# Performance work log

Hardware: AMD Instinct MI355X
Metric: run time of the kernel (lower is better)

Reference implementation:

```python
import math
import jax, jax.numpy as jnp
import numpy as np

SIZE = 5
MUL = 16                      # multiplicity of 0e and 1o in irreps_in and irreps_out
DIM = 4 * MUL                 # 16x0e (16) + 16x1o (48) = 64
INV_SQRT3 = 1.0 / math.sqrt(3.0)          # nonzero entries of wigner_3j for (1,1,0),(0,1,1),(1,0,1)
ALPHA_0 = math.sqrt(1.0 / (2 * MUL))      # out 0e: ir.dim=1 / (two uvw paths, 16*1 elements each)
ALPHA_1 = math.sqrt(3.0 / (2 * MUL))      # out 1o: ir.dim=3 / (two uvw paths, 16*1 elements each)


def _lattice():
    # torch.linspace(-1,1,size), meshgrid 'ij'; steps=(1,1,1) keeps the full cube
    r = np.linspace(-1.0, 1.0, SIZE, dtype=np.float32)
    gx, gy, gz = np.meshgrid(r, r, r, indexing='ij')
    lat = np.stack([gx, gy, gz], axis=-1)                      # (S,S,S,3), order (x,y,z)
    d = np.linalg.norm(lat, axis=-1)
    unit = np.where(d[..., None] > 0, lat / np.maximum(d[..., None], 1e-12), 0.0)
    # e3nn spherical harmonics, normalize=True, 'component' norm; l=1 basis order (y,z,x)
    sh0 = np.ones_like(d)                                      # l=0 component-normalized
    sh1 = math.sqrt(3.0) * unit[..., [1, 2, 0]]                # (S,S,S,3)
    return jnp.asarray(d), jnp.asarray(sh0), jnp.asarray(sh1)


def soft_one_hot_linspace(x, start, end, number):
    sigma = (end - start) / (number - 1)
    values = jnp.linspace(start, end, number, dtype=x.dtype)
    return jnp.exp(-(((x[..., None] - values) / sigma) ** 2)) / 1.12


def setup_inputs() -> dict:
    key = jax.random.key(0)
    k1, k2, k3, k4 = jax.random.split(key, 4)
    return {
        'x': jax.random.normal(k1, (2, DIM, 64, 64, 64), dtype=jnp.float32),
        'lin_w0': jax.random.normal(k2, (MUL, MUL), dtype=jnp.float32),
        'lin_w1': jax.random.normal(k3, (MUL, MUL), dtype=jnp.float32),
        'tp_weight': jax.random.normal(k4, (SIZE, 4 * MUL * MUL), dtype=jnp.float32),
    }


def reference(x, lin_w0, lin_w1, tp_weight):
    d, sh0, sh1 = _lattice()
    B, _, X, Y, Z = x.shape

    # ---- self connection: e3nn Linear per irrep, scaled by 1/sqrt(fan_in) ----
    inv = 1.0 / math.sqrt(MUL)
    x0 = x[:, :MUL]                                            # (B,16,X,Y,Z) scalars
    x1 = x[:, MUL:].reshape(B, MUL, 3, X, Y, Z)                # (B,16,3,X,Y,Z) vectors
    sc0 = jnp.einsum('uw,buxyz->bwxyz', lin_w0, x0) * inv
    sc1 = jnp.einsum('uw,buixyz->bwixyz', lin_w1, x1) * inv
    sc = jnp.concatenate([sc0, sc1.reshape(B, 3 * MUL, X, Y, Z)], axis=1)

    # ---- radial weights: soft one-hot embedding @ learned weights ----
    emb = soft_one_hot_linspace(d, 0.0, 1.0, SIZE) @ tp_weight                 # (S,S,S,1024)
    emb = emb * (jnp.cos(math.pi * d) / SIZE ** 1.5)[..., None]
    mm = MUL * MUL
    wA = emb[..., 0 * mm:1 * mm].reshape(SIZE, SIZE, SIZE, MUL, MUL)  # 0e(x)0e->0e
    wB = emb[..., 1 * mm:2 * mm].reshape(SIZE, SIZE, SIZE, MUL, MUL)  # 0e(x)1o->1o
    wC = emb[..., 2 * mm:3 * mm].reshape(SIZE, SIZE, SIZE, MUL, MUL)  # 1o(x)0e->1o
    wD = emb[..., 3 * mm:4 * mm].reshape(SIZE, SIZE, SIZE, MUL, MUL)  # 1o(x)1o->0e

    # ---- tp.right(sh, weight): kernel (S,S,S, in_dim, out_dim) ----
    eye3 = jnp.eye(3, dtype=x.dtype)
    k00 = ALPHA_0 * wA * sh0[..., None, None]                                        # (g,16,16)
    k10 = (ALPHA_0 * INV_SQRT3) * jnp.einsum('...uw,...i->...uiw', wD, sh1)          # (g,16,3,16)
    k01 = (ALPHA_1 * INV_SQRT3) * jnp.einsum('...uw,...k->...uwk', wB, sh1)          # (g,16,16,3)
    k11 = (ALPHA_1 * INV_SQRT3) * jnp.einsum('...uw,ik->...uiwk',
                                             wC * sh0[..., None, None], eye3)        # (g,16,3,16,3)
    g = (SIZE, SIZE, SIZE)
    top = jnp.concatenate([k00, k01.reshape(*g, MUL, 3 * MUL)], axis=-1)             # (g,16,64)
    bot = jnp.concatenate([k10.reshape(*g, 3 * MUL, MUL),
                           k11.reshape(*g, 3 * MUL, 3 * MUL)], axis=-1)              # (g,48,64)
    kernel = jnp.concatenate([top, bot], axis=-2)                                     # (S,S,S,64,64)

    # einsum('xyzio->oixyz') then conv3d (cross-correlation, same as torch)
    kernel_oi = jnp.transpose(kernel, (4, 3, 0, 1, 2))
    p = SIZE // 2
    conv = jax.lax.conv_general_dilated(
        x, kernel_oi, window_strides=(1, 1, 1), padding=[(p, p)] * 3,
        dimension_numbers=('NCDHW', 'OIDHW', 'NCDHW'))
    return sc + 0.1 * conv
```

## Files before the change

### kernel.cpp

```cpp
#include <hip/hip_runtime.h>
#include <hip/hip_bf16.h>
#include <math.h>

typedef __bf16 bf16x8 __attribute__((ext_vector_type(8)));
typedef __bf16 bf16x2 __attribute__((ext_vector_type(2)));
typedef float  f32x4  __attribute__((ext_vector_type(4)));

#define CI_STRIDE 262144
#define B_STRIDE  16777216
#define Z2 68
#define CP 40

__global__ __launch_bounds__(256) void gen_w(const float* __restrict__ tp,
                                             const float* __restrict__ lw0,
                                             const float* __restrict__ lw1,
                                             __bf16* __restrict__ Wb) {
    const int t  = blockIdx.x;
    const int dx = t / 25, dy = (t / 5) % 5, dz = t % 5;
    const float rx = -1.f + 0.5f * (float)dx;
    const float ry = -1.f + 0.5f * (float)dy;
    const float rz = -1.f + 0.5f * (float)dz;
    const float d    = sqrtf(rx * rx + ry * ry + rz * rz);
    const float invd = (d > 0.f) ? (1.f / d) : 0.f;
    const float SQRT3 = 1.7320508075688772f;
    const float sh1_0 = SQRT3 * ry * invd;
    const float sh1_1 = SQRT3 * rz * invd;
    const float sh1_2 = SQRT3 * rx * invd;
    float basis[5];
#pragma unroll
    for (int m = 0; m < 5; ++m) {
        float u = (d - 0.25f * (float)m) * 4.0f;
        basis[m] = expf(-u * u) * (1.0f / 1.12f);
    }
    const float S  = cosf(3.14159265358979323846f * d) * (1.0f / 11.180339887498949f);
    const float fA = 0.1f * 0.17677669529663687f * S;
    const float fB = 0.1f * 0.3061862178478972f * 0.5773502691896258f * S;
    const float fC = 0.1f * 0.17677669529663687f * 0.5773502691896258f * S;
    const float fD = fB;

    for (int e = threadIdx.x; e < 4096; e += 256) {
        const int co = e >> 6, ci = e & 63;
        int   tt;
        float f;
        if (ci < 16) {
            if (co < 16) { tt = ci * 16 + co; f = fA; }
            else {
                const int c = co - 16, w = c / 3, kk = c % 3;
                tt = 256 + ci * 16 + w;
                f  = fB * ((kk == 0) ? sh1_0 : (kk == 1) ? sh1_1 : sh1_2);
            }
        } else {
            const int a = ci - 16, uu = a / 3, ii = a % 3;
            const float s1i = (ii == 0) ? sh1_0 : (ii == 1) ? sh1_1 : sh1_2;
            if (co < 16) { tt = 768 + uu * 16 + co; f = fC * s1i; }
            else {
                const int c = co - 16, w = c / 3, kk = c % 3;
                tt = 512 + uu * 16 + w;
                f  = (ii == kk) ? fD : 0.0f;
            }
        }
        float E = 0.f;
#pragma unroll
        for (int m = 0; m < 5; ++m) E += basis[m] * tp[m * 1024 + tt];
        float val = f * E;
        if (t == 62) {
            if (ci < 16 && co < 16) {
                val += 0.25f * lw0[ci * 16 + co];
            } else if (ci >= 16 && co >= 16) {
                const int a = co - 16, bq = ci - 16;
                const int wq = a / 3, iq = a % 3, uq = bq / 3, iiq = bq % 3;
                if (iq == iiq) val += 0.25f * lw1[uq * 16 + wq];
            }
        }
        Wb[((size_t)(t * 2 + (ci >> 5)) * 64 + co) * 32 + (ci & 31)] = (__bf16)val;
    }
}

__global__ __launch_bounds__(512, 2) void conv_mfma(const float* __restrict__ x,
                                                    const __bf16* __restrict__ Wb,
                                                    float* __restrict__ out) {
    __shared__ __align__(16) __bf16 xs[20 * Z2 * CP];
    const int tid = threadIdx.x;
    const int l = tid & 63, w = tid >> 6;
    const int q = l >> 4, i16 = l & 15;
    const int b  = blockIdx.x >> 8;
    const int xc = (blockIdx.x >> 2) & 63;
    const int y0 = (blockIdx.x & 3) << 4;

    f32x4 acc[4][8];
#pragma unroll
    for (int mt = 0; mt < 4; ++mt)
#pragma unroll
        for (int nt = 0; nt < 8; ++nt) acc[mt][nt] = (f32x4)(0.f);

    for (int idx = tid; idx < 20 * 4 * CP; idx += 512) {
        const int r = idx / (4 * CP), rem = idx % (4 * CP);
        const int zs = rem / CP, ci = rem % CP;
        const int zp = (zs < 2) ? zs : (64 + zs);
        xs[((size_t)r * Z2 + zp) * CP + ci] = (__bf16)0.f;
    }

    const float* xb = x + (size_t)b * B_STRIDE;

    bf16x8 Acur[4], Anext[4];
#pragma unroll
    for (int mt = 0; mt < 4; ++mt)
        Acur[mt] = *(const bf16x8*)(Wb + ((size_t)(mt * 16 + i16)) * 32 + q * 8);

    for (int h = 0; h < 2; ++h) {
        for (int dx = 0; dx < 5; ++dx) {
            __syncthreads();
            {
                const int xp = xc + dx - 2;
                const bool xok = (xp >= 0) && (xp < 64);
                for (int r = w; r < 20; r += 8) {
                    const int yp = y0 + r - 2;
                    const bool ok = xok && (yp >= 0) && (yp < 64);
                    const float* src = xb + (size_t)(h * 32) * CI_STRIDE
                                     + (size_t)xp * 4096 + yp * 64 + l;
                    __bf16* dst = xs + ((size_t)r * Z2 + 2 + l) * CP;
                    if (ok) {
#pragma unroll
                        for (int ci = 0; ci < 32; ci += 2) {
                            const float a0 = src[(size_t)ci * CI_STRIDE];
                            const float a1 = src[(size_t)(ci + 1) * CI_STRIDE];
                            bf16x2 pk = {(__bf16)a0, (__bf16)a1};
                            *(bf16x2*)(dst + ci) = pk;
                        }
                    } else {
                        bf16x2 zz = {(__bf16)0.f, (__bf16)0.f};
#pragma unroll
                        for (int ci = 0; ci < 32; ci += 2) *(bf16x2*)(dst + ci) = zz;
                    }
                }
            }
            __syncthreads();

            for (int dydz = 0; dydz < 25; ++dydz) {
                const int t = dx * 25 + dydz;
                const int s = h * 125 + t;
                {
                    const int sn = (s < 249) ? (s + 1) : s;
                    const int hn = sn / 125, tn = sn % 125;
                    const __bf16* wp = Wb + ((size_t)(tn * 2 + hn) * 64 + i16) * 32 + q * 8;
#pragma unroll
                    for (int mt = 0; mt < 4; ++mt)
                        Anext[mt] = *(const bf16x8*)(wp + (size_t)mt * 16 * 32);
                }
                const int dy = dydz / 5, dz = dydz % 5;
                const __bf16* bbase = xs + ((size_t)(2 * w + dy) * Z2 + dz + i16) * CP + q * 8;
                bf16x8 Bf[8];
#pragma unroll
                for (int yy = 0; yy < 2; ++yy)
#pragma unroll
                    for (int zt = 0; zt < 4; ++zt)
                        Bf[yy * 4 + zt] = *(const bf16x8*)(bbase + (size_t)(yy * Z2 + zt * 16) * CP);
#pragma unroll
                for (int mt = 0; mt < 4; ++mt)
#pragma unroll
                    for (int nt = 0; nt < 8; ++nt)
                        acc[mt][nt] = __builtin_amdgcn_mfma_f32_16x16x32_bf16(
                            Acur[mt], Bf[nt], acc[mt][nt], 0, 0, 0);
#pragma unroll
                for (int mt = 0; mt < 4; ++mt) Acur[mt] = Anext[mt];
            }
        }
    }

    const size_t ob = (size_t)b * B_STRIDE + (size_t)xc * 4096;
#pragma unroll
    for (int mt = 0; mt < 4; ++mt)
#pragma unroll
        for (int j = 0; j < 4; ++j) {
            const int co = mt * 16 + q * 4 + j;
            float* op = out + ob + (size_t)co * CI_STRIDE;
#pragma unroll
            for (int nt = 0; nt < 8; ++nt) {
                const int y = y0 + 2 * w + (nt >> 2);
                const int z = (nt & 3) * 16 + i16;
                op[y * 64 + z] = acc[mt][nt][j];
            }
        }
}

extern "C" void kernel_launch(void* const* d_in, const int* in_sizes, int n_in,
                              void* d_out, int out_size, void* d_ws, size_t ws_size,
                              hipStream_t stream) {
    (void)in_sizes; (void)n_in; (void)out_size; (void)ws_size;
    const float* x   = (const float*)d_in[0];
    const float* lw0 = (const float*)d_in[1];
    const float* lw1 = (const float*)d_in[2];
    const float* tp  = (const float*)d_in[3];
    float* out = (float*)d_out;
    __bf16* Wb = (__bf16*)d_ws;

    gen_w<<<125, 256, 0, stream>>>(tp, lw0, lw1, Wb);
    conv_mfma<<<512, 512, 0, stream>>>(x, Wb, out);
}
```

Before: 570.2 us.

## Halve conv block to 4 waves over 8 y-rows, vectorize staging, raise MFMA priority

The conv kernel now launches 1024 blocks of 256 threads, each covering 8 y-rows with a 12-row LDS halo instead of 16 rows with a 20-row halo. This doubles the block count and shrinks LDS per block, which should help occupancy and load balance. The cost is a larger halo fraction and more redundant global reads. Staging now packs 8 channels into one 16-byte LDS store, and s_setprio is raised around the MFMA loop so compute waves are favoured over loaders.

Measured after the change: 567.5 us. Within noise of the previous version (-0.5%).

```diff
diff --git a/kernel.cpp b/kernel.cpp
--- a/kernel.cpp
+++ b/kernel.cpp
@@ -10,6 +10,7 @@
 #define B_STRIDE  16777216
 #define Z2 68
 #define CP 40
+#define NROW 12
 
 __global__ __launch_bounds__(256) void gen_w(const float* __restrict__ tp,
                                              const float* __restrict__ lw0,
@@ -76,16 +77,16 @@
     }
 }
 
-__global__ __launch_bounds__(512, 2) void conv_mfma(const float* __restrict__ x,
+__global__ __launch_bounds__(256, 2) void conv_mfma(const float* __restrict__ x,
                                                     const __bf16* __restrict__ Wb,
                                                     float* __restrict__ out) {
-    __shared__ __align__(16) __bf16 xs[20 * Z2 * CP];
+    __shared__ __align__(16) __bf16 xs[NROW * Z2 * CP];
     const int tid = threadIdx.x;
     const int l = tid & 63, w = tid >> 6;
     const int q = l >> 4, i16 = l & 15;
-    const int b  = blockIdx.x >> 8;
-    const int xc = (blockIdx.x >> 2) & 63;
-    const int y0 = (blockIdx.x & 3) << 4;
+    const int b  = blockIdx.x >> 9;
+    const int xc = (blockIdx.x >> 3) & 63;
+    const int y0 = (blockIdx.x & 7) << 3;
 
     f32x4 acc[4][8];
 #pragma unroll
@@ -93,11 +94,13 @@
 #pragma unroll
         for (int nt = 0; nt < 8; ++nt) acc[mt][nt] = (f32x4)(0.f);
 
-    for (int idx = tid; idx < 20 * 4 * CP; idx += 512) {
-        const int r = idx / (4 * CP), rem = idx % (4 * CP);
-        const int zs = rem / CP, ci = rem % CP;
+    if (tid < NROW * 4 * 4) {
+        const int r = tid >> 4, rem = tid & 15;
+        const int zs = rem >> 2, c8 = (rem & 3) << 3;
         const int zp = (zs < 2) ? zs : (64 + zs);
-        xs[((size_t)r * Z2 + zp) * CP + ci] = (__bf16)0.f;
+        bf16x8 zz = {(__bf16)0.f, (__bf16)0.f, (__bf16)0.f, (__bf16)0.f,
+                     (__bf16)0.f, (__bf16)0.f, (__bf16)0.f, (__bf16)0.f};
+        *(bf16x8*)(xs + ((size_t)r * Z2 + zp) * CP + c8) = zz;
     }
 
     const float* xb = x + (size_t)b * B_STRIDE;
@@ -113,7 +116,7 @@
             {
                 const int xp = xc + dx - 2;
                 const bool xok = (xp >= 0) && (xp < 64);
-                for (int r = w; r < 20; r += 8) {
+                for (int r = w; r < NROW; r += 4) {
                     const int yp = y0 + r - 2;
                     const bool ok = xok && (yp >= 0) && (yp < 64);
                     const float* src = xb + (size_t)(h * 32) * CI_STRIDE
@@ -121,16 +124,18 @@
                     __bf16* dst = xs + ((size_t)r * Z2 + 2 + l) * CP;
                     if (ok) {
 #pragma unroll
-                        for (int ci = 0; ci < 32; ci += 2) {
-                            const float a0 = src[(size_t)ci * CI_STRIDE];
-                            const float a1 = src[(size_t)(ci + 1) * CI_STRIDE];
-                            bf16x2 pk = {(__bf16)a0, (__bf16)a1};
-                            *(bf16x2*)(dst + ci) = pk;
+                        for (int c0 = 0; c0 < 32; c0 += 8) {
+                            bf16x8 pk;
+#pragma unroll
+                            for (int j = 0; j < 8; ++j)
+                                pk[j] = (__bf16)src[(size_t)(c0 + j) * CI_STRIDE];
+                            *(bf16x8*)(dst + c0) = pk;
                         }
                     } else {
-                        bf16x2 zz = {(__bf16)0.f, (__bf16)0.f};
-#pragma unroll
-                        for (int ci = 0; ci < 32; ci += 2) *(bf16x2*)(dst + ci) = zz;
+                        bf16x8 zz = {(__bf16)0.f, (__bf16)0.f, (__bf16)0.f, (__bf16)0.f,
+                                     (__bf16)0.f, (__bf16)0.f, (__bf16)0.f, (__bf16)0.f};
+#pragma unroll
+                        for (int c0 = 0; c0 < 32; c0 += 8) *(bf16x8*)(dst + c0) = zz;
                     }
                 }
             }
@@ -155,12 +160,14 @@
 #pragma unroll
                     for (int zt = 0; zt < 4; ++zt)
                         Bf[yy * 4 + zt] = *(const bf16x8*)(bbase + (size_t)(yy * Z2 + zt * 16) * CP);
+                __builtin_amdgcn_s_setprio(1);
 #pragma unroll
                 for (int mt = 0; mt < 4; ++mt)
 #pragma unroll
                     for (int nt = 0; nt < 8; ++nt)
                         acc[mt][nt] = __builtin_amdgcn_mfma_f32_16x16x32_bf16(
                             Acur[mt], Bf[nt], acc[mt][nt], 0, 0, 0);
+                __builtin_amdgcn_s_setprio(0);
 #pragma unroll
                 for (int mt = 0; mt < 4; ++mt) Acur[mt] = Anext[mt];
             }
@@ -195,5 +202,5 @@
     __bf16* Wb = (__bf16*)d_ws;
 
     gen_w<<<125, 256, 0, stream>>>(tp, lw0, lw1, Wb);
-    conv_mfma<<<512, 512, 0, stream>>>(x, Wb, out);
+    conv_mfma<<<1024, 256, 0, stream>>>(x, Wb, out);
 }
```
